# Performance work log

Measured on AMD Instinct MI355X. Metric: run time of the kernel, lower is better.

Reference implementation:

```python
import jax, jax.numpy as jnp
import numpy as np


def setup_inputs() -> dict:
    key = jax.random.key(0)
    ks = jax.random.split(key, 7)
    B, T, D, H = 32, 512, 512, 512
    return {
        "x": jax.random.normal(ks[0], (B, T, D), dtype=jnp.float32),
        "W_Du": jax.random.normal(ks[1], (D, H), dtype=jnp.float32) * (1.0 / np.sqrt(D)),
        "W_Dr1": jax.random.normal(ks[2], (D, H), dtype=jnp.float32) * (1.0 / np.sqrt(D)),
        "W_Dr2": jax.random.normal(ks[3], (D, H), dtype=jnp.float32) * (1.0 / np.sqrt(D)),
        "b_Du": jax.random.normal(ks[4], (H,), dtype=jnp.float32) * 0.02,
        "b_Dr1": jax.random.normal(ks[5], (H,), dtype=jnp.float32) * 0.02,
        "b_Dr2": jax.random.normal(ks[6], (H,), dtype=jnp.float32) * 0.02,
    }


def reference(x, W_Du, W_Dr1, W_Dr2, b_Du, b_Dr1, b_Dr2):
    # Precompute all per-step projections across time (batched matmuls),
    # then run the strictly sequential gated recurrence with lax.scan.
    r1 = jax.nn.softmax(jnp.einsum('btd,dh->bth', x, W_Dr1) + b_Dr1, axis=-1)  # [B,T,H]
    r2 = jax.nn.softmax(jnp.einsum('btd,dh->bth', x, W_Dr2) + b_Dr2, axis=-1)  # [B,T,H]
    u = jnp.tanh(jnp.einsum('btd,dh->bth', x, W_Du) + b_Du)                     # [B,T,H]

    def step(s, inp):
        r1t, r2t, ut = inp
        s_new = r1t * s + r2t * ut
        return s_new, s_new

    init = jnp.zeros((x.shape[0], W_Du.shape[1]), dtype=x.dtype)
    # time-major for scan: [T,B,H]
    _, ys = jax.lax.scan(
        step, init,
        (jnp.swapaxes(r1, 0, 1), jnp.swapaxes(r2, 0, 1), jnp.swapaxes(u, 0, 1)),
    )
    return jnp.swapaxes(ys, 0, 1)  # [B,T,H]
```

## Files before the change

### kernel.cpp

```cpp
#include <hip/hip_runtime.h>
#include <hip/hip_bf16.h>

#define B_N 32
#define T_N 512
#define D_N 512
#define H_N 512
#define M_N (B_N * T_N)

typedef __attribute__((ext_vector_type(8))) short bf16x8;
typedef __attribute__((ext_vector_type(4))) float f32x4;

__device__ __forceinline__ unsigned short f2bf(float f) {
  unsigned u = __float_as_uint(f);
  u += 0x7FFFu + ((u >> 16) & 1u);
  return (unsigned short)(u >> 16);
}
__device__ __forceinline__ float bf2f(unsigned short h) {
  return __uint_as_float(((unsigned)h) << 16);
}

#define GLOAD16(g, l) __builtin_amdgcn_global_load_lds( \
    (const __attribute__((address_space(1))) void*)(g), \
    (__attribute__((address_space(3))) void*)(l), 16, 0, 0)

__global__ void prep_kernel(const float* __restrict__ x,
                            const float* __restrict__ W0,
                            const float* __restrict__ W1,
                            const float* __restrict__ W2,
                            unsigned short* __restrict__ xb,
                            unsigned short* __restrict__ Wt) {
  int blk = blockIdx.x;
  int tid = threadIdx.x;
  if (blk < 768) {
    __shared__ float tile[32][33];
    int id = blk >> 8;
    int t = blk & 255;
    int kr = (t >> 4) << 5;
    int nc = (t & 15) << 5;
    const float* W = (id == 0) ? W0 : (id == 1) ? W1 : W2;
    unsigned short* Wo = Wt + (size_t)id * (D_N * H_N);
    int tx = tid & 31, ty0 = tid >> 5;
    for (int ty = ty0; ty < 32; ty += 8)
      tile[ty][tx] = W[(size_t)(kr + ty) * H_N + nc + tx];
    __syncthreads();
    for (int ty = ty0; ty < 32; ty += 8)
      Wo[(size_t)(nc + ty) * D_N + kr + tx] = f2bf(tile[tx][ty]);
  } else {
    int b = blk - 768;
    const float4* xv = (const float4*)x;
#pragma unroll
    for (int u = 0; u < 4; ++u) {
      int i = b * 1024 + u * 256 + tid;
      float4 v = xv[i];
      ushort4 o;
      o.x = f2bf(v.x); o.y = f2bf(v.y); o.z = f2bf(v.z); o.w = f2bf(v.w);
      ((ushort4*)xb)[i] = o;
    }
  }
}

__global__ __launch_bounds__(512) void gemm_act(
    const unsigned short* __restrict__ xb,
    const unsigned short* __restrict__ Wt,
    const float* __restrict__ bDu,
    const float* __restrict__ bDr1,
    const float* __restrict__ bDr2,
    float* __restrict__ uP,
    unsigned short* __restrict__ r1P,
    unsigned short* __restrict__ r2P) {
  __shared__ __align__(16) char smem[147456];

  const int tid = threadIdx.x;
  const int lane = tid & 63;
  const int wv = tid >> 6;
  const int g = lane >> 4;
  const int c16 = lane & 15;

  const int m0 = blockIdx.x * 64;
  const int id = blockIdx.y;
  const unsigned short* Wp = Wt + (size_t)id * (D_N * H_N);

  f32x4 acc[4][4];
#pragma unroll
  for (int mt = 0; mt < 4; ++mt)
#pragma unroll
    for (int nt = 0; nt < 4; ++nt)
      acc[mt][nt] = (f32x4){0.f, 0.f, 0.f, 0.f};

  const int sl = ((lane & 7) ^ (lane >> 3)) << 3;
  const unsigned short* aSrc =
      xb + (size_t)(m0 + wv * 8 + (lane >> 3)) * D_N + sl;
  const unsigned short* bSrc0 =
      Wp + (size_t)(wv * 64 + (lane >> 3)) * D_N + sl;
  const int aDst = wv * 1024;
  const int bDst = wv * 8192;

#define STAGE(buf, kstep) do {                                          \
    const int k0_ = (kstep) * 64;                                       \
    GLOAD16(aSrc + k0_, smem + (buf) * 8192 + aDst);                    \
    _Pragma("unroll")                                                   \
    for (int jj = 0; jj < 8; ++jj)                                      \
      GLOAD16(bSrc0 + jj * 4096 + k0_,                                  \
              smem + 16384 + (buf) * 65536 + bDst + jj * 1024);         \
  } while (0)

#define COMPUTE(buf) do {                                               \
    _Pragma("unroll")                                                   \
    for (int kh = 0; kh < 2; ++kh) {                                    \
      bf16x8 af[4], bb[4];                                              \
      _Pragma("unroll")                                                 \
      for (int mt = 0; mt < 4; ++mt) {                                  \
        int r = mt * 16 + c16;                                          \
        af[mt] = *(const bf16x8*)(smem + (buf) * 8192 + r * 128 +       \
                                  (((kh * 4 + g) ^ (r & 7)) << 4));     \
      }                                                                 \
      _Pragma("unroll")                                                 \
      for (int nt = 0; nt < 4; ++nt) {                                  \
        int n = wv * 64 + nt * 16 + c16;                                \
        bb[nt] = *(const bf16x8*)(smem + 16384 + (buf) * 65536 +        \
                                  n * 128 +                             \
                                  (((kh * 4 + g) ^ (n & 7)) << 4));     \
      }                                                                 \
      _Pragma("unroll")                                                 \
      for (int mt = 0; mt < 4; ++mt)                                    \
        _Pragma("unroll")                                               \
        for (int nt = 0; nt < 4; ++nt)                                  \
          acc[mt][nt] = __builtin_amdgcn_mfma_f32_16x16x32_bf16(        \
              af[mt], bb[nt], acc[mt][nt], 0, 0, 0);                    \
    }                                                                   \
  } while (0)

  STAGE(0, 0);
#pragma unroll
  for (int kk = 0; kk < 8; kk += 2) {
    asm volatile("s_waitcnt vmcnt(0)" ::: "memory");
    __syncthreads();
    STAGE(1, kk + 1);
    COMPUTE(0);
    asm volatile("s_waitcnt vmcnt(0)" ::: "memory");
    __syncthreads();
    if (kk + 2 < 8) STAGE(0, kk + 2);
    COMPUTE(1);
  }

  const int colbase = wv * 64;
  const float* bp = (id == 0) ? bDu : (id == 1) ? bDr1 : bDr2;
  float bias[4];
#pragma unroll
  for (int nt = 0; nt < 4; ++nt) bias[nt] = bp[colbase + nt * 16 + c16];

  if (id == 0) {
#pragma unroll
    for (int mt = 0; mt < 4; ++mt)
#pragma unroll
      for (int i = 0; i < 4; ++i) {
        int row = m0 + mt * 16 + g * 4 + i;
        float* op = uP + (size_t)row * H_N + colbase + c16;
#pragma unroll
        for (int nt = 0; nt < 4; ++nt)
          op[nt * 16] = tanhf(acc[mt][nt][i] + bias[nt]);
      }
  } else {
    float* red  = (float*)smem;
    float* red2 = (float*)(smem + 2048);
    unsigned short* rP = (id == 1) ? r1P : r2P;
#pragma unroll
    for (int mt = 0; mt < 4; ++mt)
#pragma unroll
      for (int i = 0; i < 4; ++i) {
        float m = -3.0e38f;
#pragma unroll
        for (int nt = 0; nt < 4; ++nt) m = fmaxf(m, acc[mt][nt][i] + bias[nt]);
        m = fmaxf(m, __shfl_xor(m, 1));
        m = fmaxf(m, __shfl_xor(m, 2));
        m = fmaxf(m, __shfl_xor(m, 4));
        m = fmaxf(m, __shfl_xor(m, 8));
        if (c16 == 0) red[(mt * 16 + g * 4 + i) * 8 + wv] = m;
      }
    __syncthreads();
#pragma unroll
    for (int mt = 0; mt < 4; ++mt)
#pragma unroll
      for (int i = 0; i < 4; ++i) {
        int rl = mt * 16 + g * 4 + i;
        float4 q0 = *(const float4*)(red + rl * 8);
        float4 q1 = *(const float4*)(red + rl * 8 + 4);
        float m = fmaxf(fmaxf(fmaxf(q0.x, q0.y), fmaxf(q0.z, q0.w)),
                        fmaxf(fmaxf(q1.x, q1.y), fmaxf(q1.z, q1.w)));
        float s = 0.f;
#pragma unroll
        for (int nt = 0; nt < 4; ++nt) {
          float e = __expf(acc[mt][nt][i] + bias[nt] - m);
          acc[mt][nt][i] = e;
          s += e;
        }
        s += __shfl_xor(s, 1);
        s += __shfl_xor(s, 2);
        s += __shfl_xor(s, 4);
        s += __shfl_xor(s, 8);
        if (c16 == 0) red2[rl * 8 + wv] = s;
      }
    __syncthreads();
#pragma unroll
    for (int mt = 0; mt < 4; ++mt)
#pragma unroll
      for (int i = 0; i < 4; ++i) {
        int rl = mt * 16 + g * 4 + i;
        float4 q0 = *(const float4*)(red2 + rl * 8);
        float4 q1 = *(const float4*)(red2 + rl * 8 + 4);
        float inv = 1.f / (q0.x + q0.y + q0.z + q0.w + q1.x + q1.y + q1.z + q1.w);
        unsigned short* op = rP + (size_t)(m0 + rl) * H_N + colbase + c16;
#pragma unroll
        for (int nt = 0; nt < 4; ++nt)
          op[nt * 16] = f2bf(acc[mt][nt][i] * inv);
      }
  }
#undef STAGE
#undef COMPUTE
}

__global__ void scan_pass1(const unsigned short* __restrict__ r1P,
                           const unsigned short* __restrict__ r2P,
                           const float* __restrict__ uP,
                           float* __restrict__ cP,
                           float* __restrict__ cS) {
  int gt = blockIdx.x * 256 + threadIdx.x;
  int chunk = gt >> 14;
  int r = gt & 16383;
  int b = r >> 9, h = r & 511;
  size_t idx = (size_t)b * (T_N * H_N) + (size_t)(chunk * 64) * H_N + h;
  float p = 1.f, s = 0.f;
#pragma unroll 4
  for (int j = 0; j < 64; ++j) {
    float a = bf2f(r1P[idx]);
    float c = bf2f(r2P[idx]);
    float uu = uP[idx];
    s = fmaf(a, s, c * uu);
    p *= a;
    idx += H_N;
  }
  cP[gt] = p;
  cS[gt] = s;
}

__global__ void scan_pass3(const unsigned short* __restrict__ r1P,
                           const unsigned short* __restrict__ r2P,
                           const float* __restrict__ uP,
                           const float* __restrict__ cP,
                           const float* __restrict__ cS,
                           float* __restrict__ out) {
  int gt = blockIdx.x * 256 + threadIdx.x;
  int chunk = gt >> 14;
  int r = gt & 16383;
  int b = r >> 9, h = r & 511;
  float s = 0.f;
  for (int c2 = 0; c2 < chunk; ++c2)
    s = fmaf(cP[c2 * 16384 + r], s, cS[c2 * 16384 + r]);
  size_t idx = (size_t)b * (T_N * H_N) + (size_t)(chunk * 64) * H_N + h;
#pragma unroll 4
  for (int j = 0; j < 64; ++j) {
    float a = bf2f(r1P[idx]);
    float c = bf2f(r2P[idx]);
    float uu = uP[idx];
    s = fmaf(a, s, c * uu);
    out[idx] = s;
    idx += H_N;
  }
}

extern "C" void kernel_launch(void* const* d_in, const int* in_sizes, int n_in,
                              void* d_out, int out_size, void* d_ws, size_t ws_size,
                              hipStream_t stream) {
  const float* x  = (const float*)d_in[0];
  const float* W0 = (const float*)d_in[1];
  const float* W1 = (const float*)d_in[2];
  const float* W2 = (const float*)d_in[3];
  const float* b0 = (const float*)d_in[4];
  const float* b1 = (const float*)d_in[5];
  const float* b2 = (const float*)d_in[6];
  float* out = (float*)d_out;

  char* ws = (char*)d_ws;
  unsigned short* xb  = (unsigned short*)ws;
  unsigned short* Wt  = (unsigned short*)(ws + 16777216);
  float*          uP  = (float*)(ws + 18350080);
  unsigned short* r1P = (unsigned short*)(ws + 51904512);
  unsigned short* r2P = (unsigned short*)(ws + 68681728);
  float*          cP  = (float*)(ws + 85458944);
  float*          cS  = (float*)(ws + 85983232);

  prep_kernel<<<2816, 256, 0, stream>>>(x, W0, W1, W2, xb, Wt);
  gemm_act<<<dim3(256, 3), 512, 0, stream>>>(xb, Wt, b0, b1, b2, uP, r1P, r2P);
  scan_pass1<<<512, 256, 0, stream>>>(r1P, r2P, uP, cP, cS);
  scan_pass3<<<512, 256, 0, stream>>>(r1P, r2P, uP, cP, cS, out);
}
```

Measured before the change: 96.85 us.

## Halve GEMM k-tile to shrink LDS and restructure double-buffered pipeline

The GEMM k-step drops from 64 to 32, which cuts shared memory from 144KB to 76KB and changes the swizzle to fit 64-byte rows. The main loop now issues the next stage's loads before waiting on a partial vmcnt, so global loads overlap the MFMA work, and it wraps the MFMA sequence in setprio. The smaller LDS footprint lets more blocks share a CU, but the loop now runs twice as many iterations, each with two barriers, which adds synchronisation overhead. The softmax reduction scratch moves to a region past the buffers.

Measured after the change: 123.6 us. +27.6%, slower.

```diff
diff --git a/kernel.cpp b/kernel.cpp
--- a/kernel.cpp
+++ b/kernel.cpp
@@ -59,7 +59,7 @@
   }
 }
 
-__global__ __launch_bounds__(512) void gemm_act(
+__global__ __launch_bounds__(512, 4) void gemm_act(
     const unsigned short* __restrict__ xb,
     const unsigned short* __restrict__ Wt,
     const float* __restrict__ bDu,
@@ -68,7 +68,7 @@
     float* __restrict__ uP,
     unsigned short* __restrict__ r1P,
     unsigned short* __restrict__ r2P) {
-  __shared__ __align__(16) char smem[147456];
+  __shared__ __align__(16) char smem[77824];
 
   const int tid = threadIdx.x;
   const int lane = tid & 63;
@@ -87,60 +87,59 @@
     for (int nt = 0; nt < 4; ++nt)
       acc[mt][nt] = (f32x4){0.f, 0.f, 0.f, 0.f};
 
-  const int sl = ((lane & 7) ^ (lane >> 3)) << 3;
-  const unsigned short* aSrc =
-      xb + (size_t)(m0 + wv * 8 + (lane >> 3)) * D_N + sl;
-  const unsigned short* bSrc0 =
-      Wp + (size_t)(wv * 64 + (lane >> 3)) * D_N + sl;
-  const int aDst = wv * 1024;
-  const int bDst = wv * 8192;
+  const int nb = wv * 64 + (lane >> 2);
+  const int sb = (lane & 3) ^ ((nb >> 1) & 3);
+  const unsigned short* bSrc = Wp + (size_t)nb * D_N + sb * 8;
+  const int na = (wv & 3) * 16 + (lane >> 2);
+  const int sa = (lane & 3) ^ ((na >> 1) & 3);
+  const unsigned short* aSrc = xb + (size_t)(m0 + na) * D_N + sa * 8;
+
+  const int sr = (g ^ ((c16 >> 1) & 3)) << 4;
 
 #define STAGE(buf, kstep) do {                                          \
-    const int k0_ = (kstep) * 64;                                       \
-    GLOAD16(aSrc + k0_, smem + (buf) * 8192 + aDst);                    \
-    _Pragma("unroll")                                                   \
-    for (int jj = 0; jj < 8; ++jj)                                      \
-      GLOAD16(bSrc0 + jj * 4096 + k0_,                                  \
-              smem + 16384 + (buf) * 65536 + bDst + jj * 1024);         \
+    const int k0_ = (kstep) * 32;                                       \
+    _Pragma("unroll")                                                   \
+    for (int jj = 0; jj < 4; ++jj)                                      \
+      GLOAD16(bSrc + (size_t)jj * (16 * D_N) + k0_,                     \
+              smem + 8192 + (buf) * 32768 + wv * 4096 + jj * 1024);     \
+    if (wv < 4)                                                         \
+      GLOAD16(aSrc + k0_, smem + (buf) * 4096 + wv * 1024);             \
   } while (0)
 
 #define COMPUTE(buf) do {                                               \
-    _Pragma("unroll")                                                   \
-    for (int kh = 0; kh < 2; ++kh) {                                    \
-      bf16x8 af[4], bb[4];                                              \
+    bf16x8 af[4], bb[4];                                                \
+    _Pragma("unroll")                                                   \
+    for (int mt = 0; mt < 4; ++mt)                                      \
+      af[mt] = *(const bf16x8*)(smem + (buf) * 4096 +                   \
+                                (mt * 16 + c16) * 64 + sr);             \
+    _Pragma("unroll")                                                   \
+    for (int nt = 0; nt < 4; ++nt)                                      \
+      bb[nt] = *(const bf16x8*)(smem + 8192 + (buf) * 32768 +           \
+                                (wv * 64 + nt * 16 + c16) * 64 + sr);   \
+    __builtin_amdgcn_s_setprio(1);                                      \
+    _Pragma("unroll")                                                   \
+    for (int mt = 0; mt < 4; ++mt)                                      \
       _Pragma("unroll")                                                 \
-      for (int mt = 0; mt < 4; ++mt) {                                  \
-        int r = mt * 16 + c16;                                          \
-        af[mt] = *(const bf16x8*)(smem + (buf) * 8192 + r * 128 +       \
-                                  (((kh * 4 + g) ^ (r & 7)) << 4));     \
-      }                                                                 \
-      _Pragma("unroll")                                                 \
-      for (int nt = 0; nt < 4; ++nt) {                                  \
-        int n = wv * 64 + nt * 16 + c16;                                \
-        bb[nt] = *(const bf16x8*)(smem + 16384 + (buf) * 65536 +        \
-                                  n * 128 +                             \
-                                  (((kh * 4 + g) ^ (n & 7)) << 4));     \
-      }                                                                 \
-      _Pragma("unroll")                                                 \
-      for (int mt = 0; mt < 4; ++mt)                                    \
-        _Pragma("unroll")                                               \
-        for (int nt = 0; nt < 4; ++nt)                                  \
-          acc[mt][nt] = __builtin_amdgcn_mfma_f32_16x16x32_bf16(        \
-              af[mt], bb[nt], acc[mt][nt], 0, 0, 0);                    \
-    }                                                                   \
+      for (int nt = 0; nt < 4; ++nt)                                    \
+        acc[mt][nt] = __builtin_amdgcn_mfma_f32_16x16x32_bf16(          \
+            af[mt], bb[nt], acc[mt][nt], 0, 0, 0);                      \
+    __builtin_amdgcn_s_setprio(0);                                      \
   } while (0)
 
   STAGE(0, 0);
 #pragma unroll
-  for (int kk = 0; kk < 8; kk += 2) {
-    asm volatile("s_waitcnt vmcnt(0)" ::: "memory");
-    __syncthreads();
-    STAGE(1, kk + 1);
-    COMPUTE(0);
-    asm volatile("s_waitcnt vmcnt(0)" ::: "memory");
-    __syncthreads();
-    if (kk + 2 < 8) STAGE(0, kk + 2);
-    COMPUTE(1);
+  for (int t = 0; t < 16; ++t) {
+    const int buf = t & 1;
+    if (t < 15) {
+      STAGE(buf ^ 1, t + 1);
+      if (wv < 4) asm volatile("s_waitcnt vmcnt(5)" ::: "memory");
+      else        asm volatile("s_waitcnt vmcnt(4)" ::: "memory");
+    } else {
+      asm volatile("s_waitcnt vmcnt(0)" ::: "memory");
+    }
+    __syncthreads();
+    COMPUTE(buf);
+    __syncthreads();
   }
 
   const int colbase = wv * 64;
@@ -161,8 +160,8 @@
           op[nt * 16] = tanhf(acc[mt][nt][i] + bias[nt]);
       }
   } else {
-    float* red  = (float*)smem;
-    float* red2 = (float*)(smem + 2048);
+    float* red  = (float*)(smem + 73728);
+    float* red2 = red + 512;
     unsigned short* rP = (id == 1) ? r1P : r2P;
 #pragma unroll
     for (int mt = 0; mt < 4; ++mt)
```
